# Kernel optimization log

Measured on AMD Instinct MI355X. Metric: run time of the kernel, lower is better.

Reference implementation:

```python
import jax, jax.numpy as jnp
import numpy as np

B, T = 4096, 2048
C_MCC, C_TR = 100, 50
EPS = 1e-9


def setup_inputs() -> dict:
    key = jax.random.key(0)
    k1, k2, k3, k4 = jax.random.split(key, 4)
    amount = jax.random.normal(k1, (B, T), dtype=jnp.float32)
    # category 0 is the padding token, masked out by (1 - ohe[0]); draw from [1, C)
    mcc = jax.random.randint(k2, (B, T), 1, C_MCC, dtype=jnp.int32)
    tr_type = jax.random.randint(k3, (B, T), 1, C_TR, dtype=jnp.int32)
    seq_lens = jax.random.randint(k4, (B,), 1, T + 1, dtype=jnp.int32)
    return {"amount": amount, "mcc": mcc, "tr_type": tr_type, "seq_lens": seq_lens}


def _cat_aggs(cat, val, C):
    """Per-(batch,category) count / mean / std of val, via scatter-add.
    Equivalent to the torch one-hot-matmul formulation but without the
    [B,T,C] one-hot intermediate."""
    Bb, Tt = cat.shape
    flat = (jnp.arange(Bb)[:, None] * C + cat).reshape(-1)  # [B*T]
    z = jnp.zeros(Bb * C, dtype=val.dtype)
    cnt = z.at[flat].add(1.0).reshape(Bb, C)                 # ohe.sum(dim=1)
    s = z.at[flat].add(val.reshape(-1)).reshape(Bb, C)       # (ohe*val).sum(dim=1)
    ss = z.at[flat].add((val * val).reshape(-1)).reshape(Bb, C)
    mask = (jnp.arange(C) > 0).astype(val.dtype)[None, :]    # 1 - ohe[0]
    e_cnt = cnt * mask
    e_mean = s / (e_cnt + EPS)
    a = jnp.clip(ss - s * s / (e_cnt + EPS), 0.0)
    e_std = jnp.sqrt(a / (jnp.clip(e_cnt - 1.0, 0.0) + EPS))
    return e_cnt, e_mean, e_std


def _forward(amount, mcc, tr_type, seq_lens):
    sl = seq_lens.astype(amount.dtype)
    processed = [sl[:, None]]
    # numeric column aggregates (was_logified=False path)
    s = amount.sum(axis=1)
    mean_ = s / (sl + EPS)
    a = jnp.clip((amount * amount).sum(axis=1) - s * s / (sl + EPS), 0.0)
    std_ = jnp.sqrt(a / (jnp.clip(sl - 1.0, 0.0) + EPS))
    processed += [s[:, None], mean_[:, None], std_[:, None]]
    distinct = []
    for cat, C in ((mcc, C_MCC), (tr_type, C_TR)):
        e_cnt, e_mean, e_std = _cat_aggs(cat, amount, C)
        processed += [e_cnt, e_mean, e_std]
        # e_cnt.gt(0).float().sum(dim=1, keepdim=True)
        distinct.append((e_cnt > 0.0).astype(amount.dtype).sum(axis=1, keepdims=True))
    return jnp.concatenate(processed + distinct, axis=1)  # [B, 456]


def reference(amount, mcc, tr_type, seq_lens):
    return _forward(amount, mcc, tr_type, seq_lens)
```

## Files before the change

### kernel.cpp

```cpp
#include <hip/hip_runtime.h>
#include <stdint.h>


#define NCOL 456
static constexpr float EPS = 1e-9f;

typedef __bf16 bf16x8 __attribute__((ext_vector_type(8)));
typedef float  f32x4  __attribute__((ext_vector_type(4)));
typedef int    i32x8  __attribute__((ext_vector_type(8)));
typedef unsigned int u32x4 __attribute__((ext_vector_type(4)));
typedef short  s16x2  __attribute__((ext_vector_type(2)));

__device__ __forceinline__ uint32_t hw_eqmask(uint32_t h) {
    const uint32_t s = 0x80008000u - h;
    const s16x2 m = __builtin_bit_cast(s16x2, s) >> 15;
    return __builtin_bit_cast(uint32_t, m);
}

__global__ __launch_bounds__(512, 4) void agg_fused(
    const float4* __restrict__ a4,
    const int4* __restrict__ m4,
    const int4* __restrict__ t4,
    const int* __restrict__ seq_lens,
    float* __restrict__ out, int B)
{
    const int tid  = threadIdx.x;
    const int lane = tid & 63;
    const int wv   = tid >> 6;

    __shared__ uint32_t lv[2048];
    __shared__ uint32_t lm[2048];
    __shared__ uint32_t lt[2048];
    __shared__ float part[4][2][3][176];
    __shared__ float scw[4][8][2];

    const size_t base4 = (size_t)blockIdx.x * 2048;
#pragma unroll
    for (int j = 0; j < 4; ++j) {
        const size_t gi = base4 + (size_t)j * 512 + tid;
        const float4 a = a4[gi];
        const int4   m = m4[gi];
        const int4   t = t4[gi];

        uint32_t w = __builtin_amdgcn_cvt_pk_fp8_f32(a.x, a.y, 0u, false);
        w = __builtin_amdgcn_cvt_pk_fp8_f32(a.z, a.w, w, true);
        lv[j * 512 + tid] = w;
        lm[j * 512 + tid] = (uint32_t)m.x | ((uint32_t)m.y << 8)
                          | ((uint32_t)m.z << 16) | ((uint32_t)m.w << 24);
        lt[j * 512 + tid] = (uint32_t)t.x | ((uint32_t)t.y << 8)
                          | ((uint32_t)t.z << 16) | ((uint32_t)t.w << 24);

        float s = (a.x + a.y) + (a.z + a.w);
        float q = fmaf(a.x, a.x, fmaf(a.y, a.y, fmaf(a.z, a.z, a.w * a.w)));
#pragma unroll
        for (int off = 32; off; off >>= 1) {
            s += __shfl_xor(s, off, 64);
            q += __shfl_xor(q, off, 64);
        }
        if (lane == 0) { scw[j][wv][0] = s; scw[j][wv][1] = q; }
    }
    __syncthreads();

    const int rl   = wv >> 1;
    const int half = wv & 1;
    const int row  = blockIdx.x * 4 + rl;
    const int n    = lane & 15;
    const int grp  = lane >> 4;
    const bool istr = (grp >= 2);
    const int ntc  = istr ? ((n - 7) & 15) : n;
    const uint32_t patB = (uint32_t)(((ntc << 4) | n) * 0x01010101u);

    const int bb = rl * 2048 + half * 1024 + ((grp & 1) << 5);
    const uint8_t* pv = (const uint8_t*)lv + bb;
    const uint8_t* pk = (const uint8_t*)(istr ? lt : lm) + bb;

    f32x4 accC = {0.f,0.f,0.f,0.f};
    f32x4 accS = {0.f,0.f,0.f,0.f};
    f32x4 accQ = {0.f,0.f,0.f,0.f};

#pragma unroll 2
    for (int st = 0; st < 16; ++st) {
        const int off = st << 6;
        const uint4 v0 = *reinterpret_cast<const uint4*>(pv + off);
        const uint4 v1 = *reinterpret_cast<const uint4*>(pv + off + 16);
        const uint4 k0 = *reinterpret_cast<const uint4*>(pk + off);
        const uint4 k1 = *reinterpret_cast<const uint4*>(pk + off + 16);

        i32x8 fA1, fAa, fB1, fBa;
#define DOW(j, kw, vw) { \
        const uint32_t kx = (kw) ^ patB; \
        const uint32_t hu = kx & 0x0f0f0f0fu; \
        const uint32_t mu = (((0x80808080u - hu) & 0x80808080u) >> 7) * 255u; \
        const uint32_t ht = (kx >> 4) & 0x0f0f0f0fu; \
        const uint32_t mt = (((0x80808080u - ht) & 0x80808080u) >> 7) * 255u; \
        fA1[j] = (int)(mt & 0x38383838u);   \
        fAa[j] = (int)(mt & (vw)); \
        fB1[j] = (int)(mu & 0x38383838u); \
        fBa[j] = (int)(mu & (vw)); }
        DOW(0, k0.x, v0.x) DOW(1, k0.y, v0.y) DOW(2, k0.z, v0.z) DOW(3, k0.w, v0.w)
        DOW(4, k1.x, v1.x) DOW(5, k1.y, v1.y) DOW(6, k1.z, v1.z) DOW(7, k1.w, v1.w)
#undef DOW

        accC = __builtin_amdgcn_mfma_scale_f32_16x16x128_f8f6f4(
                   fA1, fB1, accC, 0, 0, 0, 0x7f7f7f7f, 0, 0x7f7f7f7f);
        accS = __builtin_amdgcn_mfma_scale_f32_16x16x128_f8f6f4(
                   fA1, fBa, accS, 0, 0, 0, 0x7f7f7f7f, 0, 0x7f7f7f7f);
        accQ = __builtin_amdgcn_mfma_scale_f32_16x16x128_f8f6f4(
                   fAa, fBa, accQ, 0, 0, 0, 0x7f7f7f7f, 0, 0x7f7f7f7f);
    }

    {
        float* my = &part[rl][half][0][0];
#pragma unroll
        for (int r = 0; r < 4; ++r) {
            const int rr = grp * 4 + r;
            int addr = -1;
            if (rr <= 6)       addr = rr * 16 + n;
            else if (rr <= 10) addr = 112 + (rr - 7) * 16 + n;
            if (addr >= 0) {
                my[addr]       = accC[r];
                my[176 + addr] = accS[r];
                my[352 + addr] = accQ[r];
            }
        }
    }
    __syncthreads();

    auto TB = [&](int s, int c) -> float {
        return part[rl][0][s][c] + part[rl][1][s][c];
    };

    int dm = 0, dt = 0;
    if (half) {
        for (int c0 = 0; c0 < 160; c0 += 64) {
            const int c = c0 + lane;
            bool pos = false;
            if (c >= 1 && c < 100)        pos = TB(0, c) > 0.f;
            else if (c >= 101 && c < 150) pos = TB(0, 112 + (c - 100)) > 0.f;
            dm += __popcll(__ballot(pos && c < 100));
            dt += __popcll(__ballot(pos && c >= 100));
        }
    }

    float s_tot = 0.f, ss_tot = 0.f;
#pragma unroll
    for (int w = 0; w < 8; ++w) {
        s_tot  += scw[rl][w][0];
        ss_tot += scw[rl][w][1];
    }
    const float sl = (float)seq_lens[row];
    float* orow = out + (size_t)row * NCOL;

    for (int cc = lane; cc < 228; cc += 64) {
        const int col = half * 228 + cc;
        float v;
        if (col == 0)      v = sl;
        else if (col == 1) v = s_tot;
        else if (col == 2) v = s_tot / (sl + EPS);
        else if (col == 3) {
            float a = fmaxf(ss_tot - s_tot * s_tot / (sl + EPS), 0.f);
            v = sqrtf(a / (fmaxf(sl - 1.f, 0.f) + EPS));
        }
        else if (col == 454) v = (float)dm;
        else if (col == 455) v = (float)dt;
        else {
            int base, C, toff;
            if (col < 304) { base = 4;   C = 100; toff = 0;   }
            else           { base = 304; C = 50;  toff = 112; }
            const int rel   = col - base;
            const int which = rel / C;
            const int c     = rel - which * C;
            const float cnt = (c > 0) ? TB(0, toff + c) : 0.f;
            const float sc  = TB(1, toff + c);
            const float ssc = TB(2, toff + c);
            if (which == 0)      v = cnt;
            else if (which == 1) v = sc / (cnt + EPS);
            else {
                float a = fmaxf(ssc - sc * sc / (cnt + EPS), 0.f);
                v = sqrtf(a / (fmaxf(cnt - 1.f, 0.f) + EPS));
            }
        }
        orow[col] = v;
    }
}

__global__ __launch_bounds__(512, 8) void agg2d_legacy(
    const float* __restrict__ amount,
    const int* __restrict__ mcc,
    const int* __restrict__ tr,
    const int* __restrict__ seq_lens,
    float* __restrict__ out, int T, int B)
{
    const int lane = threadIdx.x & 63;
    const int wv   = threadIdx.x >> 6;
    const int rl   = wv >> 1;
    const int half = wv & 1;
    const int row  = blockIdx.x * 4 + rl;
    const int n    = lane & 15;
    const int grp  = lane >> 4;
    const bool istr = (grp >= 2);
    const int ntc  = istr ? ((n - 7) & 15) : n;
    const uint32_t xorpat = (uint32_t)(((ntc << 4) | n) * 0x00010001u);
    const int roff = (grp & 1) * 8;

    __shared__ float part[4][2][3][176];
    __shared__ float scal[4][2][2];

    const int hb = half * (T >> 1);
    const float* pa = amount + (size_t)row * T + hb + roff;
    const int*   pk = (istr ? tr : mcc) + (size_t)row * T + hb + roff;

    f32x4 accC = {0.f,0.f,0.f,0.f};
    f32x4 accS = {0.f,0.f,0.f,0.f};
    f32x4 accQ = {0.f,0.f,0.f,0.f};

    const int nstep = T >> 5;
#pragma unroll 2
    for (int st = 0; st < nstep; ++st) {
        const int base = st << 4;
        const float4 a0 = *reinterpret_cast<const float4*>(pa + base);
        const float4 a1 = *reinterpret_cast<const float4*>(pa + base + 4);
        const int4   k0 = *reinterpret_cast<const int4*>(pk + base);
        const int4   k1 = *reinterpret_cast<const int4*>(pk + base + 4);

        const float av[8] = {a0.x,a0.y,a0.z,a0.w,a1.x,a1.y,a1.z,a1.w};
        const uint32_t kv[8] = {(uint32_t)k0.x,(uint32_t)k0.y,(uint32_t)k0.z,(uint32_t)k0.w,
                                (uint32_t)k1.x,(uint32_t)k1.y,(uint32_t)k1.z,(uint32_t)k1.w};

        u32x4 wA1, wAa, wB1, wBa;
#pragma unroll
        for (int i = 0; i < 4; ++i) {
            const uint32_t kpk = __builtin_amdgcn_perm(kv[2*i+1], kv[2*i], 0x05040100u);
            const uint32_t kx  = kpk ^ xorpat;
            const uint32_t mu  = hw_eqmask(kx & 0x000f000fu);
            const uint32_t mt  = hw_eqmask((kx >> 4) & 0x000f000fu);
            const uint32_t apk = __builtin_amdgcn_perm(
                __float_as_uint(av[2*i+1]), __float_as_uint(av[2*i]), 0x07060302u);
            wA1[i] = mt & 0x3f803f80u;
            wAa[i] = mt & apk;
            wB1[i] = mu & 0x3f803f80u;
            wBa[i] = mu & apk;
        }
        const bf16x8 fA1 = __builtin_bit_cast(bf16x8, wA1);
        const bf16x8 fAa = __builtin_bit_cast(bf16x8, wAa);
        const bf16x8 fB1 = __builtin_bit_cast(bf16x8, wB1);
        const bf16x8 fBa = __builtin_bit_cast(bf16x8, wBa);

        accC = __builtin_amdgcn_mfma_f32_16x16x32_bf16(fA1, fB1, accC, 0, 0, 0);
        accS = __builtin_amdgcn_mfma_f32_16x16x32_bf16(fA1, fBa, accS, 0, 0, 0);
        accQ = __builtin_amdgcn_mfma_f32_16x16x32_bf16(fAa, fBa, accQ, 0, 0, 0);
    }

    {
        float* my = &part[rl][half][0][0];
#pragma unroll
        for (int r = 0; r < 4; ++r) {
            const int rr = grp * 4 + r;
            int addr = -1;
            if (rr <= 6)       addr = rr * 16 + n;
            else if (rr <= 10) addr = 112 + (rr - 7) * 16 + n;
            if (addr >= 0) {
                my[addr]       = accC[r];
                my[176 + addr] = accS[r];
                my[352 + addr] = accQ[r];
            }
        }
    }
    float sS = 0.f, sQ = 0.f;
    if (grp == 0) {
        sS = accS[0] + accS[1] + accS[2] + accS[3];
        sQ = accQ[0] + accQ[1] + accQ[2] + accQ[3];
    } else if (grp == 1) {
        sS = accS[0] + accS[1] + accS[2];
        sQ = accQ[0] + accQ[1] + accQ[2];
    }
#pragma unroll
    for (int off = 32; off; off >>= 1) {
        sS += __shfl_xor(sS, off, 64);
        sQ += __shfl_xor(sQ, off, 64);
    }
    if (lane == 0) { scal[rl][half][0] = sS; scal[rl][half][1] = sQ; }
    __syncthreads();

    auto TB = [&](int s, int c) -> float {
        return part[rl][0][s][c] + part[rl][1][s][c];
    };

    int dm = 0, dt = 0;
    if (half) {
        for (int c0 = 0; c0 < 160; c0 += 64) {
            const int c = c0 + lane;
            bool pos = false;
            if (c >= 1 && c < 100)        pos = TB(0, c) > 0.f;
            else if (c >= 101 && c < 150) pos = TB(0, 112 + (c - 100)) > 0.f;
            dm += __popcll(__ballot(pos && c < 100));
            dt += __popcll(__ballot(pos && c >= 100));
        }
    }

    const float sl     = (float)seq_lens[row];
    const float s_tot  = scal[rl][0][0] + scal[rl][1][0];
    const float ss_tot = scal[rl][0][1] + scal[rl][1][1];
    float* orow = out + (size_t)row * NCOL;

    for (int cc = lane; cc < 228; cc += 64) {
        const int col = half * 228 + cc;
        float v;
        if (col == 0)      v = sl;
        else if (col == 1) v = s_tot;
        else if (col == 2) v = s_tot / (sl + EPS);
        else if (col == 3) {
            float a = fmaxf(ss_tot - s_tot * s_tot / (sl + EPS), 0.f);
            v = sqrtf(a / (fmaxf(sl - 1.f, 0.f) + EPS));
        }
        else if (col == 454) v = (float)dm;
        else if (col == 455) v = (float)dt;
        else {
            int base, C, toff;
            if (col < 304) { base = 4;   C = 100; toff = 0;   }
            else           { base = 304; C = 50;  toff = 112; }
            const int rel   = col - base;
            const int which = rel / C;
            const int c     = rel - which * C;
            const float cnt = (c > 0) ? TB(0, toff + c) : 0.f;
            const float sc  = TB(1, toff + c);
            const float ssc = TB(2, toff + c);
            if (which == 0)      v = cnt;
            else if (which == 1) v = sc / (cnt + EPS);
            else {
                float a = fmaxf(ssc - sc * sc / (cnt + EPS), 0.f);
                v = sqrtf(a / (fmaxf(cnt - 1.f, 0.f) + EPS));
            }
        }
        orow[col] = v;
    }
}

extern "C" void kernel_launch(void* const* d_in, const int* in_sizes, int n_in,
                              void* d_out, int out_size, void* d_ws, size_t ws_size,
                              hipStream_t stream) {
    const float* amount   = (const float*)d_in[0];
    const int*   mcc      = (const int*)d_in[1];
    const int*   tr_type  = (const int*)d_in[2];
    const int*   seq_lens = (const int*)d_in[3];
    float*       out      = (float*)d_out;

    const int B = in_sizes[3];
    const int T = in_sizes[0] / B;

    if (T == 2048 && (B % 4) == 0) {
        agg_fused<<<B / 4, 512, 0, stream>>>(
            (const float4*)amount, (const int4*)mcc, (const int4*)tr_type,
            seq_lens, out, B);
    } else {
        agg2d_legacy<<<B / 4, 512, 0, stream>>>(amount, mcc, tr_type, seq_lens, out, T, B);
    }
}
```

Before: 51.98 us.

## Restructure fused aggregation to one wave per row with per-wave LDS staging

The fused kernel now assigns one 64-lane wave per batch row and uses 256-thread blocks. Each wave stages half a row at a time into its own LDS region, then runs the MFMA one-hot accumulation over it. This removes block-wide __syncthreads and the cross-wave partial-table merge, and packs category bytes with v_perm. In exchange each wave carries the full row serially with less parallelism per row, and it relies on wave-local LDS ordering without block barriers.

```diff
diff --git a/kernel.cpp b/kernel.cpp
--- a/kernel.cpp
+++ b/kernel.cpp
@@ -17,7 +17,17 @@
     return __builtin_bit_cast(uint32_t, m);
 }
 
-__global__ __launch_bounds__(512, 4) void agg_fused(
+__device__ __forceinline__ uint32_t pack_lobytes(int4 m) {
+    const uint32_t p01 = __builtin_amdgcn_perm((uint32_t)m.y, (uint32_t)m.x, 0x00000400u);
+    const uint32_t p23 = __builtin_amdgcn_perm((uint32_t)m.w, (uint32_t)m.z, 0x00000400u);
+    return __builtin_amdgcn_perm(p23, p01, 0x05040100u);
+}
+
+#define WSTR 784
+#define MOFF 256
+#define TOFF 528
+
+__global__ __launch_bounds__(256, 8) void agg_fused(
     const float4* __restrict__ a4,
     const int4* __restrict__ m4,
     const int4* __restrict__ t4,
@@ -27,40 +37,151 @@
     const int tid  = threadIdx.x;
     const int lane = tid & 63;
     const int wv   = tid >> 6;
-
-    __shared__ uint32_t lv[2048];
-    __shared__ uint32_t lm[2048];
-    __shared__ uint32_t lt[2048];
-    __shared__ float part[4][2][3][176];
-    __shared__ float scw[4][8][2];
-
-    const size_t base4 = (size_t)blockIdx.x * 2048;
-#pragma unroll
-    for (int j = 0; j < 4; ++j) {
-        const size_t gi = base4 + (size_t)j * 512 + tid;
-        const float4 a = a4[gi];
-        const int4   m = m4[gi];
-        const int4   t = t4[gi];
-
-        uint32_t w = __builtin_amdgcn_cvt_pk_fp8_f32(a.x, a.y, 0u, false);
-        w = __builtin_amdgcn_cvt_pk_fp8_f32(a.z, a.w, w, true);
-        lv[j * 512 + tid] = w;
-        lm[j * 512 + tid] = (uint32_t)m.x | ((uint32_t)m.y << 8)
-                          | ((uint32_t)m.z << 16) | ((uint32_t)m.w << 24);
-        lt[j * 512 + tid] = (uint32_t)t.x | ((uint32_t)t.y << 8)
-                          | ((uint32_t)t.z << 16) | ((uint32_t)t.w << 24);
-
-        float s = (a.x + a.y) + (a.z + a.w);
-        float q = fmaf(a.x, a.x, fmaf(a.y, a.y, fmaf(a.z, a.z, a.w * a.w)));
-#pragma unroll
-        for (int off = 32; off; off >>= 1) {
-            s += __shfl_xor(s, off, 64);
-            q += __shfl_xor(q, off, 64);
-        }
-        if (lane == 0) { scw[j][wv][0] = s; scw[j][wv][1] = q; }
-    }
-    __syncthreads();
-
+    const int row  = blockIdx.x * 4 + wv;
+    const int n    = lane & 15;
+    const int grp  = lane >> 4;
+    const bool istr = (grp >= 2);
+    const int ntc  = istr ? ((n - 7) & 15) : n;
+    const uint32_t patB = (uint32_t)(((ntc << 4) | n) * 0x01010101u);
+
+    __shared__ uint32_t smem[4 * WSTR];
+    uint32_t* ws = smem + wv * WSTR;
+
+    f32x4 accC = {0.f,0.f,0.f,0.f};
+    f32x4 accS = {0.f,0.f,0.f,0.f};
+    f32x4 accQ = {0.f,0.f,0.f,0.f};
+    float s_p = 0.f, q_p = 0.f;
+
+    const uint8_t* pv = (const uint8_t*)ws + ((grp & 1) << 5);
+    const uint8_t* pk = (const uint8_t*)(ws + (istr ? TOFF : MOFF)) + ((grp & 1) << 5);
+
+#pragma unroll 1
+    for (int h = 0; h < 2; ++h) {
+        const size_t g4 = (size_t)row * 512 + h * 256;
+#pragma unroll
+        for (int j = 0; j < 4; ++j) {
+            const size_t gi = g4 + j * 64 + lane;
+            const float4 a = a4[gi];
+            const int4   m = m4[gi];
+            const int4   t = t4[gi];
+            uint32_t w = __builtin_amdgcn_cvt_pk_fp8_f32(a.x, a.y, 0u, false);
+            w = __builtin_amdgcn_cvt_pk_fp8_f32(a.z, a.w, w, true);
+            ws[j * 64 + lane]        = w;
+            ws[MOFF + j * 64 + lane] = pack_lobytes(m);
+            ws[TOFF + j * 64 + lane] = pack_lobytes(t);
+            s_p += (a.x + a.y) + (a.z + a.w);
+            q_p = fmaf(a.x, a.x, fmaf(a.y, a.y, fmaf(a.z, a.z, fmaf(a.w, a.w, q_p))));
+        }
+
+#pragma unroll 2
+        for (int st = 0; st < 16; ++st) {
+            const int off = st << 6;
+            const uint4 v0 = *reinterpret_cast<const uint4*>(pv + off);
+            const uint4 v1 = *reinterpret_cast<const uint4*>(pv + off + 16);
+            const uint4 k0 = *reinterpret_cast<const uint4*>(pk + off);
+            const uint4 k1 = *reinterpret_cast<const uint4*>(pk + off + 16);
+
+            i32x8 fA1, fAa, fB1, fBa;
+#define DOW(j, kw, vw) { \
+            const uint32_t kx = (kw) ^ patB; \
+            const uint32_t hu = kx & 0x0f0f0f0fu; \
+            const uint32_t mu = (((0x80808080u - hu) & 0x80808080u) >> 7) * 255u; \
+            const uint32_t ht = (kx >> 4) & 0x0f0f0f0fu; \
+            const uint32_t mt = (((0x80808080u - ht) & 0x80808080u) >> 7) * 255u; \
+            fA1[j] = (int)(mt & 0x38383838u);   \
+            fAa[j] = (int)(mt & (vw)); \
+            fB1[j] = (int)(mu & 0x38383838u); \
+            fBa[j] = (int)(mu & (vw)); }
+            DOW(0, k0.x, v0.x) DOW(1, k0.y, v0.y) DOW(2, k0.z, v0.z) DOW(3, k0.w, v0.w)
+            DOW(4, k1.x, v1.x) DOW(5, k1.y, v1.y) DOW(6, k1.z, v1.z) DOW(7, k1.w, v1.w)
+#undef DOW
+
+            accC = __builtin_amdgcn_mfma_scale_f32_16x16x128_f8f6f4(
+                       fA1, fB1, accC, 0, 0, 0, 0x7f7f7f7f, 0, 0x7f7f7f7f);
+            accS = __builtin_amdgcn_mfma_scale_f32_16x16x128_f8f6f4(
+                       fA1, fBa, accS, 0, 0, 0, 0x7f7f7f7f, 0, 0x7f7f7f7f);
+            accQ = __builtin_amdgcn_mfma_scale_f32_16x16x128_f8f6f4(
+                       fAa, fBa, accQ, 0, 0, 0, 0x7f7f7f7f, 0, 0x7f7f7f7f);
+        }
+    }
+
+    float* tbl = (float*)ws;
+#pragma unroll
+    for (int r = 0; r < 4; ++r) {
+        const int rr = grp * 4 + r;
+        int addr = -1;
+        if (rr <= 6)       addr = rr * 16 + n;
+        else if (rr <= 10) addr = 112 + (rr - 7) * 16 + n;
+        if (addr >= 0) {
+            tbl[addr]       = accC[r];
+            tbl[176 + addr] = accS[r];
+            tbl[352 + addr] = accQ[r];
+        }
+    }
+    asm volatile("s_waitcnt lgkmcnt(0)" ::: "memory");
+    __builtin_amdgcn_sched_barrier(0);
+
+    int dm = 0, dt = 0;
+    for (int c0 = 0; c0 < 160; c0 += 64) {
+        const int c = c0 + lane;
+        bool pos = false;
+        if (c >= 1 && c < 100)        pos = tbl[c] > 0.f;
+        else if (c >= 101 && c < 150) pos = tbl[112 + (c - 100)] > 0.f;
+        dm += __popcll(__ballot(pos && c < 100));
+        dt += __popcll(__ballot(pos && c >= 100));
+    }
+
+#pragma unroll
+    for (int off = 32; off; off >>= 1) {
+        s_p += __shfl_xor(s_p, off, 64);
+        q_p += __shfl_xor(q_p, off, 64);
+    }
+    const float s_tot = s_p, ss_tot = q_p;
+    const float sl = (float)seq_lens[row];
+    float* orow = out + (size_t)row * NCOL;
+
+    for (int cc = lane; cc < NCOL; cc += 64) {
+        const int col = cc;
+        float v;
+        if (col == 0)      v = sl;
+        else if (col == 1) v = s_tot;
+        else if (col == 2) v = s_tot / (sl + EPS);
+        else if (col == 3) {
+            float a = fmaxf(ss_tot - s_tot * s_tot / (sl + EPS), 0.f);
+            v = sqrtf(a / (fmaxf(sl - 1.f, 0.f) + EPS));
+        }
+        else if (col == 454) v = (float)dm;
+        else if (col == 455) v = (float)dt;
+        else {
+            int base, C, toff;
+            if (col < 304) { base = 4;   C = 100; toff = 0;   }
+            else           { base = 304; C = 50;  toff = 112; }
+            const int rel   = col - base;
+            const int which = rel / C;
+            const int c     = rel - which * C;
+            const float cnt = (c > 0) ? tbl[toff + c] : 0.f;
+            const float sc  = tbl[176 + toff + c];
+            const float ssc = tbl[352 + toff + c];
+            if (which == 0)      v = cnt;
+            else if (which == 1) v = sc / (cnt + EPS);
+            else {
+                float a = fmaxf(ssc - sc * sc / (cnt + EPS), 0.f);
+                v = sqrtf(a / (fmaxf(cnt - 1.f, 0.f) + EPS));
+            }
+        }
+        orow[col] = v;
+    }
+}
+
+__global__ __launch_bounds__(512, 8) void agg2d_legacy(
+    const float* __restrict__ amount,
+    const int* __restrict__ mcc,
+    const int* __restrict__ tr,
+    const int* __restrict__ seq_lens,
+    float* __restrict__ out, int T, int B)
+{
+    const int lane = threadIdx.x & 63;
+    const int wv   = threadIdx.x >> 6;
     const int rl   = wv >> 1;
     const int half = wv & 1;
     const int row  = blockIdx.x * 4 + rl;
@@ -68,45 +189,55 @@
     const int grp  = lane >> 4;
     const bool istr = (grp >= 2);
     const int ntc  = istr ? ((n - 7) & 15) : n;
-    const uint32_t patB = (uint32_t)(((ntc << 4) | n) * 0x01010101u);
-
-    const int bb = rl * 2048 + half * 1024 + ((grp & 1) << 5);
-    const uint8_t* pv = (const uint8_t*)lv + bb;
-    const uint8_t* pk = (const uint8_t*)(istr ? lt : lm) + bb;
+    const uint32_t xorpat = (uint32_t)(((ntc << 4) | n) * 0x00010001u);
+    const int roff = (grp & 1) * 8;
+
+    __shared__ float part[4][2][3][176];
+    __shared__ float scal[4][2][2];
+
+    const int hb = half * (T >> 1);
+    const float* pa = amount + (size_t)row * T + hb + roff;
+    const int*   pk = (istr ? tr : mcc) + (size_t)row * T + hb + roff;
 
     f32x4 accC = {0.f,0.f,0.f,0.f};
     f32x4 accS = {0.f,0.f,0.f,0.f};
     f32x4 accQ = {0.f,0.f,0.f,0.f};
 
+    const int nstep = T >> 5;
 #pragma unroll 2
-    for (int st = 0; st < 16; ++st) {
-        const int off = st << 6;
-        const uint4 v0 = *reinterpret_cast<const uint4*>(pv + off);
-        const uint4 v1 = *reinterpret_cast<const uint4*>(pv + off + 16);
-        const uint4 k0 = *reinterpret_cast<const uint4*>(pk + off);
-        const uint4 k1 = *reinterpret_cast<const uint4*>(pk + off + 16);
-
-        i32x8 fA1, fAa, fB1, fBa;
-#define DOW(j, kw, vw) { \
-        const uint32_t kx = (kw) ^ patB; \
-        const uint32_t hu = kx & 0x0f0f0f0fu; \
-        const uint32_t mu = (((0x80808080u - hu) & 0x80808080u) >> 7) * 255u; \
-        const uint32_t ht = (kx >> 4) & 0x0f0f0f0fu; \
-        const uint32_t mt = (((0x80808080u - ht) & 0x80808080u) >> 7) * 255u; \
-        fA1[j] = (int)(mt & 0x38383838u);   \
-        fAa[j] = (int)(mt & (vw)); \
-        fB1[j] = (int)(mu & 0x38383838u); \
-        fBa[j] = (int)(mu & (vw)); }
-        DOW(0, k0.x, v0.x) DOW(1, k0.y, v0.y) DOW(2, k0.z, v0.z) DOW(3, k0.w, v0.w)
-        DOW(4, k1.x, v1.x) DOW(5, k1.y, v1.y) DOW(6, k1.z, v1.z) DOW(7, k1.w, v1.w)
-#undef DOW
-
-        accC = __builtin_amdgcn_mfma_scale_f32_16x16x128_f8f6f4(
-                   fA1, fB1, accC, 0, 0, 0, 0x7f7f7f7f, 0, 0x7f7f7f7f);
-        accS = __builtin_amdgcn_mfma_scale_f32_16x16x128_f8f6f4(
-                   fA1, fBa, accS, 0, 0, 0, 0x7f7f7f7f, 0, 0x7f7f7f7f);
-        accQ = __builtin_amdgcn_mfma_scale_f32_16x16x128_f8f6f4(
-                   fAa, fBa, accQ, 0, 0, 0, 0x7f7f7f7f, 0, 0x7f7f7f7f);
+    for (int st = 0; st < nstep; ++st) {
+        const int base = st << 4;
+        const float4 a0 = *reinterpret_cast<const float4*>(pa + base);
+        const float4 a1 = *reinterpret_cast<const float4*>(pa + base + 4);
+        const int4   k0 = *reinterpret_cast<const int4*>(pk + base);
+        const int4   k1 = *reinterpret_cast<const int4*>(pk + base + 4);
+
+        const float av[8] = {a0.x,a0.y,a0.z,a0.w,a1.x,a1.y,a1.z,a1.w};
+        const uint32_t kv[8] = {(uint32_t)k0.x,(uint32_t)k0.y,(uint32_t)k0.z,(uint32_t)k0.w,
+                                (uint32_t)k1.x,(uint32_t)k1.y,(uint32_t)k1.z,(uint32_t)k1.w};
+
+        u32x4 wA1, wAa, wB1, wBa;
+#pragma unroll
+        for (int i = 0; i < 4; ++i) {
+            const uint32_t kpk = __builtin_amdgcn_perm(kv[2*i+1], kv[2*i], 0x05040100u);
+            const uint32_t kx  = kpk ^ xorpat;
+            const uint32_t mu  = hw_eqmask(kx & 0x000f000fu);
+            const uint32_t mt  = hw_eqmask((kx >> 4) & 0x000f000fu);
+            const uint32_t apk = __builtin_amdgcn_perm(
+                __float_as_uint(av[2*i+1]), __float_as_uint(av[2*i]), 0x07060302u);
+            wA1[i] = mt & 0x3f803f80u;
+            wAa[i] = mt & apk;
+            wB1[i] = mu & 0x3f803f80u;
+            wBa[i] = mu & apk;
+        }
+        const bf16x8 fA1 = __builtin_bit_cast(bf16x8, wA1);
+        const bf16x8 fAa = __builtin_bit_cast(bf16x8, wAa);
+        const bf16x8 fB1 = __builtin_bit_cast(bf16x8, wB1);
+        const bf16x8 fBa = __builtin_bit_cast(bf16x8, wBa);
+
+        accC = __builtin_amdgcn_mfma_f32_16x16x32_bf16(fA1, fB1, accC, 0, 0, 0);
+        accS = __builtin_amdgcn_mfma_f32_16x16x32_bf16(fA1, fBa, accS, 0, 0, 0);
+        accQ = __builtin_amdgcn_mfma_f32_16x16x32_bf16(fAa, fBa, accQ, 0, 0, 0);
     }
 
     {
@@ -124,6 +255,20 @@
             }
         }
     }
+    float sS = 0.f, sQ = 0.f;
+    if (grp == 0) {
+        sS = accS[0] + accS[1] + accS[2] + accS[3];
+        sQ = accQ[0] + accQ[1] + accQ[2] + accQ[3];
+    } else if (grp == 1) {
+        sS = accS[0] + accS[1] + accS[2];
+        sQ = accQ[0] + accQ[1] + accQ[2];
+    }
+#pragma unroll
+    for (int off = 32; off; off >>= 1) {
+        sS += __shfl_xor(sS, off, 64);
+        sQ += __shfl_xor(sQ, off, 64);
+    }
+    if (lane == 0) { scal[rl][half][0] = sS; scal[rl][half][1] = sQ; }
     __syncthreads();
 
     auto TB = [&](int s, int c) -> float {
@@ -142,13 +287,9 @@
         }
     }
 
-    float s_tot = 0.f, ss_tot = 0.f;
-#pragma unroll
-    for (int w = 0; w < 8; ++w) {
-        s_tot  += scw[rl][w][0];
-        ss_tot += scw[rl][w][1];
-    }
-    const float sl = (float)seq_lens[row];
+    const float sl     = (float)seq_lens[row];
+    const float s_tot  = scal[rl][0][0] + scal[rl][1][0];
+    const float ss_tot = scal[rl][0][1] + scal[rl][1][1];
     float* orow = out + (size_t)row * NCOL;
 
     for (int cc = lane; cc < 228; cc += 64) {
@@ -184,158 +325,6 @@
     }
 }
 
-__global__ __launch_bounds__(512, 8) void agg2d_legacy(
-    const float* __restrict__ amount,
-    const int* __restrict__ mcc,
-    const int* __restrict__ tr,
-    const int* __restrict__ seq_lens,
-    float* __restrict__ out, int T, int B)
-{
-    const int lane = threadIdx.x & 63;
-    const int wv   = threadIdx.x >> 6;
-    const int rl   = wv >> 1;
-    const int half = wv & 1;
-    const int row  = blockIdx.x * 4 + rl;
-    const int n    = lane & 15;
-    const int grp  = lane >> 4;
-    const bool istr = (grp >= 2);
-    const int ntc  = istr ? ((n - 7) & 15) : n;
-    const uint32_t xorpat = (uint32_t)(((ntc << 4) | n) * 0x00010001u);
-    const int roff = (grp & 1) * 8;
-
-    __shared__ float part[4][2][3][176];
-    __shared__ float scal[4][2][2];
-
-    const int hb = half * (T >> 1);
-    const float* pa = amount + (size_t)row * T + hb + roff;
-    const int*   pk = (istr ? tr : mcc) + (size_t)row * T + hb + roff;
-
-    f32x4 accC = {0.f,0.f,0.f,0.f};
-    f32x4 accS = {0.f,0.f,0.f,0.f};
-    f32x4 accQ = {0.f,0.f,0.f,0.f};
-
-    const int nstep = T >> 5;
-#pragma unroll 2
-    for (int st = 0; st < nstep; ++st) {
-        const int base = st << 4;
-        const float4 a0 = *reinterpret_cast<const float4*>(pa + base);
-        const float4 a1 = *reinterpret_cast<const float4*>(pa + base + 4);
-        const int4   k0 = *reinterpret_cast<const int4*>(pk + base);
-        const int4   k1 = *reinterpret_cast<const int4*>(pk + base + 4);
-
-        const float av[8] = {a0.x,a0.y,a0.z,a0.w,a1.x,a1.y,a1.z,a1.w};
-        const uint32_t kv[8] = {(uint32_t)k0.x,(uint32_t)k0.y,(uint32_t)k0.z,(uint32_t)k0.w,
-                                (uint32_t)k1.x,(uint32_t)k1.y,(uint32_t)k1.z,(uint32_t)k1.w};
-
-        u32x4 wA1, wAa, wB1, wBa;
-#pragma unroll
-        for (int i = 0; i < 4; ++i) {
-            const uint32_t kpk = __builtin_amdgcn_perm(kv[2*i+1], kv[2*i], 0x05040100u);
-            const uint32_t kx  = kpk ^ xorpat;
-            const uint32_t mu  = hw_eqmask(kx & 0x000f000fu);
-            const uint32_t mt  = hw_eqmask((kx >> 4) & 0x000f000fu);
-            const uint32_t apk = __builtin_amdgcn_perm(
-                __float_as_uint(av[2*i+1]), __float_as_uint(av[2*i]), 0x07060302u);
-            wA1[i] = mt & 0x3f803f80u;
-            wAa[i] = mt & apk;
-            wB1[i] = mu & 0x3f803f80u;
-            wBa[i] = mu & apk;
-        }
-        const bf16x8 fA1 = __builtin_bit_cast(bf16x8, wA1);
-        const bf16x8 fAa = __builtin_bit_cast(bf16x8, wAa);
-        const bf16x8 fB1 = __builtin_bit_cast(bf16x8, wB1);
-        const bf16x8 fBa = __builtin_bit_cast(bf16x8, wBa);
-
-        accC = __builtin_amdgcn_mfma_f32_16x16x32_bf16(fA1, fB1, accC, 0, 0, 0);
-        accS = __builtin_amdgcn_mfma_f32_16x16x32_bf16(fA1, fBa, accS, 0, 0, 0);
-        accQ = __builtin_amdgcn_mfma_f32_16x16x32_bf16(fAa, fBa, accQ, 0, 0, 0);
-    }
-
-    {
-        float* my = &part[rl][half][0][0];
-#pragma unroll
-        for (int r = 0; r < 4; ++r) {
-            const int rr = grp * 4 + r;
-            int addr = -1;
-            if (rr <= 6)       addr = rr * 16 + n;
-            else if (rr <= 10) addr = 112 + (rr - 7) * 16 + n;
-            if (addr >= 0) {
-                my[addr]       = accC[r];
-                my[176 + addr] = accS[r];
-                my[352 + addr] = accQ[r];
-            }
-        }
-    }
-    float sS = 0.f, sQ = 0.f;
-    if (grp == 0) {
-        sS = accS[0] + accS[1] + accS[2] + accS[3];
-        sQ = accQ[0] + accQ[1] + accQ[2] + accQ[3];
-    } else if (grp == 1) {
-        sS = accS[0] + accS[1] + accS[2];
-        sQ = accQ[0] + accQ[1] + accQ[2];
-    }
-#pragma unroll
-    for (int off = 32; off; off >>= 1) {
-        sS += __shfl_xor(sS, off, 64);
-        sQ += __shfl_xor(sQ, off, 64);
-    }
-    if (lane == 0) { scal[rl][half][0] = sS; scal[rl][half][1] = sQ; }
-    __syncthreads();
-
-    auto TB = [&](int s, int c) -> float {
-        return part[rl][0][s][c] + part[rl][1][s][c];
-    };
-
-    int dm = 0, dt = 0;
-    if (half) {
-        for (int c0 = 0; c0 < 160; c0 += 64) {
-            const int c = c0 + lane;
-            bool pos = false;
-            if (c >= 1 && c < 100)        pos = TB(0, c) > 0.f;
-            else if (c >= 101 && c < 150) pos = TB(0, 112 + (c - 100)) > 0.f;
-            dm += __popcll(__ballot(pos && c < 100));
-            dt += __popcll(__ballot(pos && c >= 100));
-        }
-    }
-
-    const float sl     = (float)seq_lens[row];
-    const float s_tot  = scal[rl][0][0] + scal[rl][1][0];
-    const float ss_tot = scal[rl][0][1] + scal[rl][1][1];
-    float* orow = out + (size_t)row * NCOL;
-
-    for (int cc = lane; cc < 228; cc += 64) {
-        const int col = half * 228 + cc;
-        float v;
-        if (col == 0)      v = sl;
-        else if (col == 1) v = s_tot;
-        else if (col == 2) v = s_tot / (sl + EPS);
-        else if (col == 3) {
-            float a = fmaxf(ss_tot - s_tot * s_tot / (sl + EPS), 0.f);
-            v = sqrtf(a / (fmaxf(sl - 1.f, 0.f) + EPS));
-        }
-        else if (col == 454) v = (float)dm;
-        else if (col == 455) v = (float)dt;
-        else {
-            int base, C, toff;
-            if (col < 304) { base = 4;   C = 100; toff = 0;   }
-            else           { base = 304; C = 50;  toff = 112; }
-            const int rel   = col - base;
-            const int which = rel / C;
-            const int c     = rel - which * C;
-            const float cnt = (c > 0) ? TB(0, toff + c) : 0.f;
-            const float sc  = TB(1, toff + c);
-            const float ssc = TB(2, toff + c);
-            if (which == 0)      v = cnt;
-            else if (which == 1) v = sc / (cnt + EPS);
-            else {
-                float a = fmaxf(ssc - sc * sc / (cnt + EPS), 0.f);
-                v = sqrtf(a / (fmaxf(cnt - 1.f, 0.f) + EPS));
-            }
-        }
-        orow[col] = v;
-    }
-}
-
 extern "C" void kernel_launch(void* const* d_in, const int* in_sizes, int n_in,
                               void* d_out, int out_size, void* d_ws, size_t ws_size,
                               hipStream_t stream) {
@@ -349,7 +338,7 @@
     const int T = in_sizes[0] / B;
 
     if (T == 2048 && (B % 4) == 0) {
-        agg_fused<<<B / 4, 512, 0, stream>>>(
+        agg_fused<<<B / 4, 256, 0, stream>>>(
             (const float4*)amount, (const int4*)mcc, (const int4*)tr_type,
             seq_lens, out, B);
     } else {
```

Result: no change. 52.81 us (+1.6%).
